# Optimization experiments

Hardware: AMD Instinct MI355X
Metric: run time of the kernel (lower is better)

Reference implementation:

```python
import jax, jax.numpy as jnp
import numpy as np

L, B, S, E, H, V = 4, 2, 1024, 1024, 16, 32000
HD = E // H          # head_size = 64
FF = 6 * E           # FeedForward expansion = 6
EPS = 1e-5


def setup_inputs() -> dict:
    key = jax.random.key(0)
    ks = jax.random.split(key, 12)
    std = jnp.float32(0.02)

    def nrm(k, shape):
        return jax.random.normal(k, shape, jnp.float32) * std

    return {
        "x":   jax.random.randint(ks[0], (B, S), 0, V),
        "emb": nrm(ks[1], (V, E)),            # token embedding table
        "pos": nrm(ks[2], (S, E)),            # position embedding table (context = S)
        "Wq":  nrm(ks[3], (L, H, E, HD)),     # per-layer, per-head q Linear (no bias)
        "Wk":  nrm(ks[4], (L, H, E, HD)),
        "Wv":  nrm(ks[5], (L, H, E, HD)),
        "Wo":  nrm(ks[6], (L, E, E)),         # MHA output projection
        "g1":  jnp.ones((L, E), jnp.float32), "b1": jnp.zeros((L, E), jnp.float32),
        "g2":  jnp.ones((L, E), jnp.float32), "b2": jnp.zeros((L, E), jnp.float32),
        "W1":  nrm(ks[7], (L, E, FF)),        # FFN up
        "W2":  nrm(ks[8], (L, FF, E)),        # FFN down
        "gf":  jnp.ones((E,), jnp.float32), "bf": jnp.zeros((E,), jnp.float32),
        "Wf":  nrm(ks[9], (E, V)),            # final LM head (no bias)
    }


def _ln(x, g, b):
    mu = jnp.mean(x, -1, keepdims=True)
    var = jnp.mean((x - mu) ** 2, -1, keepdims=True)
    return (x - mu) * jax.lax.rsqrt(var + EPS) * g + b


def _gpt(x, emb, pos, Wq, Wk, Wv, Wo, g1, b1, g2, b2, W1, W2, gf, bf, Wf):
    Bsz, Sl = x.shape
    h = emb[x] + pos[:Sl]                         # [B,S,E]
    mask = jnp.tril(jnp.ones((Sl, Sl), bool))     # causal 'trill' buffer

    def block(h, p):
        wq, wk, wv, wo, ga, ba, gb, bb, w1, w2 = p
        z = _ln(h, ga, ba)
        q = jnp.einsum('bse,hed->bhsd', z, wq)
        k = jnp.einsum('bse,hed->bhsd', z, wk)
        v = jnp.einsum('bse,hed->bhsd', z, wv)
        att = jnp.einsum('bhsd,bhtd->bhst', q, k) * (HD ** -0.5)
        att = jnp.where(mask, att, -jnp.inf)
        att = jax.nn.softmax(att, axis=-1)
        o = jnp.einsum('bhst,bhtd->bhsd', att, v)
        o = o.transpose(0, 2, 1, 3).reshape(h.shape[0], h.shape[1], E)  # concat heads
        h = h + o @ wo                                                   # residual 1
        z = _ln(h, gb, bb)
        h = h + jax.nn.gelu(z @ w1, approximate=False) @ w2              # residual 2
        return h, None

    h, _ = jax.lax.scan(block, h, (Wq, Wk, Wv, Wo, g1, b1, g2, b2, W1, W2))
    return _ln(h, gf, bf) @ Wf                    # logits [B,S,V]


def reference(x, emb, pos, Wq, Wk, Wv, Wo, g1, b1, g2, b2, W1, W2, gf, bf, Wf):
    return _gpt(x, emb, pos, Wq, Wk, Wv, Wo, g1, b1, g2, b2, W1, W2, gf, bf, Wf)
```

## Files before the change

kernel.cpp:

```cpp
#include <hip/hip_runtime.h>
#include <hip/hip_bf16.h>
#include <math.h>


typedef unsigned short ushort_t;
typedef unsigned short us8 __attribute__((ext_vector_type(8)));
typedef unsigned short us4 __attribute__((ext_vector_type(4)));
typedef __bf16 bf16x8 __attribute__((ext_vector_type(8)));
typedef float f32x4 __attribute__((ext_vector_type(4)));

#define LN_EPS 1e-5f

__device__ inline ushort_t f2bf(float f) {
    union { float f; unsigned u; } v; v.f = f;
    unsigned r = v.u + 0x7FFFu + ((v.u >> 16) & 1u);
    return (ushort_t)(r >> 16);
}

__device__ inline ushort_t bf16u(float f) {
    __hip_bfloat16 h = __float2bfloat16(f);
    return *(ushort_t*)&h;
}

#define GLD_LDS16(gp, lp)                                                  \
    __builtin_amdgcn_global_load_lds(                                      \
        (const __attribute__((address_space(1))) unsigned int*)(gp),       \
        (__attribute__((address_space(3))) unsigned int*)(lp), 16, 0, 0)

enum { EPI_F32 = 0, EPI_BF16 = 1, EPI_ADDF32 = 2, EPI_GELU = 3, EPI_TBF16 = 4,
       EPI_ATOM = 5, EPI_QKV = 6 };

template<int EPI>
__global__ __launch_bounds__(512)
void gemm8ph(const ushort_t* __restrict__ A, const ushort_t* __restrict__ B,
             void* __restrict__ Cv, int mt, int K, int lda, int ldb, int ldc)
{
    extern __shared__ ushort_t smem[];

    const int nwg  = gridDim.x;
    const int orig = blockIdx.x;
    int wgid = orig;
    if (nwg >= 8) {
        const int q = nwg >> 3, r = nwg & 7;
        const int xcd = orig & 7, i = orig >> 3;
        wgid = (xcd < r ? xcd * (q + 1) : r * (q + 1) + (xcd - r) * q) + i;
    }
    const int m0 = (wgid % mt) * 256;
    const int n0 = (wgid / mt) * 256;

    const int tid  = threadIdx.x;
    const int lane = tid & 63;
    const int wid  = tid >> 6;
    const int wm   = wid >> 2, wn = wid & 3;
    const int cg   = lane >> 4, cl = lane & 15;

    const int nt = K >> 6;
    const int ni = nt >> 1;

    auto stageA = [&](int t, int h) {
        ushort_t* dst = smem + (t & 1) * 32768 + h * 8192;
        const int k0 = t * 64;
        #pragma unroll
        for (int q = 0; q < 2; ++q) {
            const int slot = q * 512 + tid;
            const int r = slot >> 3, pc = slot & 7;
            const int col = (pc ^ (r & 7)) * 8;
            GLD_LDS16(&A[(long)(m0 + h * 128 + r) * lda + k0 + col], dst + slot * 8);
        }
    };
    auto stageB = [&](int t, int h) {
        ushort_t* dst = smem + (t & 1) * 32768 + 16384 + h * 8192;
        const int k0 = t * 64;
        #pragma unroll
        for (int q = 0; q < 2; ++q) {
            const int slot = q * 512 + tid;
            const int r = slot >> 3, pc = slot & 7;
            const int col = (pc ^ (r & 7)) * 8;
            GLD_LDS16(&B[(long)(n0 + h * 128 + r) * ldb + k0 + col], dst + slot * 8);
        }
    };

    stageA(0, 0); stageA(0, 1);
    stageB(0, 0); stageB(0, 1);
    stageB(1, 0); stageB(1, 1);
    asm volatile("s_waitcnt vmcnt(4)" ::: "memory");
    __builtin_amdgcn_s_barrier();

    f32x4 acc[8][4] = {};
    bf16x8 breg[4][2];

    for (int i = 0; i < ni; ++i) {
        const int te = 2 * i, to = te + 1;
        const bool nl = (i + 1 < ni);

        #pragma unroll
        for (int p = 0; p < 8; ++p) {
            const int t = (p < 4) ? te : to;
            const int q = p & 3;
            const ushort_t* Ar = smem + (t & 1) * 32768;
            const ushort_t* Br = Ar + 16384;

            if (q == 0) {
                #pragma unroll
                for (int nf = 0; nf < 4; ++nf) {
                    const int rb = wn * 64 + nf * 16 + cl;
                    #pragma unroll
                    for (int kk = 0; kk < 2; ++kk)
                        breg[nf][kk] = __builtin_bit_cast(bf16x8, *(const us8*)&Br[
                            rb * 64 + (((kk * 4 + cg) ^ (rb & 7)) * 8)]);
                }
            }
            bf16x8 af[2][2];
            #pragma unroll
            for (int mi = 0; mi < 2; ++mi) {
                const int ra = wm * 128 + q * 32 + mi * 16 + cl;
                #pragma unroll
                for (int kk = 0; kk < 2; ++kk)
                    af[mi][kk] = __builtin_bit_cast(bf16x8, *(const us8*)&Ar[
                        ra * 64 + (((kk * 4 + cg) ^ (ra & 7)) * 8)]);
            }

            if (p == 0)      { stageA(to, 0); }
            else if (p == 1) { stageA(to, 1); if (nl) stageB(te + 2, 0); }
            else if (p == 2) { if (nl) stageB(te + 2, 1); }
            else if (p == 4) { if (nl) stageA(te + 2, 0); }
            else if (p == 5) { if (nl) stageA(te + 2, 1); }
            else if (p == 6) { if (nl) stageB(to + 2, 0); }
            else if (p == 7) { if (nl) stageB(to + 2, 1); }

            __builtin_amdgcn_s_barrier();
            asm volatile("s_waitcnt lgkmcnt(0)" ::: "memory");
            __builtin_amdgcn_s_setprio(1);
            #pragma unroll
            for (int mi = 0; mi < 2; ++mi)
                #pragma unroll
                for (int nf = 0; nf < 4; ++nf)
                    #pragma unroll
                    for (int kk = 0; kk < 2; ++kk)
                        acc[q * 2 + mi][nf] = __builtin_amdgcn_mfma_f32_16x16x32_bf16(
                            af[mi][kk], breg[nf][kk], acc[q * 2 + mi][nf], 0, 0, 0);
            __builtin_amdgcn_s_setprio(0);

            if (p == 3) {
                if (nl) asm volatile("s_waitcnt vmcnt(4)" ::: "memory");
                else    asm volatile("s_waitcnt vmcnt(0)" ::: "memory");
            } else if (p == 7 && nl) {
                asm volatile("s_waitcnt vmcnt(4)" ::: "memory");
            }
            __builtin_amdgcn_s_barrier();
        }
    }

    if (EPI == EPI_F32) {
        float* lds_f = (float*)smem;
        #pragma unroll
        for (int c = 0; c < 2; ++c) {
            #pragma unroll
            for (int mf4 = 0; mf4 < 4; ++mf4) {
                #pragma unroll
                for (int nf = 0; nf < 4; ++nf) {
                    const int scol = (wn * 64 + nf * 16 + cl) ^ (cg << 4);
                    #pragma unroll
                    for (int r = 0; r < 4; ++r) {
                        const int lrow = wm * 64 + mf4 * 16 + cg * 4 + r;
                        lds_f[lrow * 256 + scol] = acc[c * 4 + mf4][nf][r];
                    }
                }
            }
            __builtin_amdgcn_s_barrier();
            #pragma unroll
            for (int rr = 0; rr < 16; ++rr) {
                const int lrow = wid * 16 + rr;
                const int rowg = m0 + (lrow >> 6) * 128 + c * 64 + (lrow & 63);
                const int lcol = (lane * 4) ^ ((((lrow >> 2) & 3)) << 4);
                const f32x4 v  = *(const f32x4*)&lds_f[lrow * 256 + lane * 4];
                *(f32x4*)&((float*)Cv)[(long)rowg * ldc + n0 + lcol] = v;
            }
            if (c == 0) __builtin_amdgcn_s_barrier();
        }
        return;
    }

    const int rb = m0 + wm * 128 + cg * 4;
    const int cb = n0 + wn * 64 + cl;

    #pragma unroll
    for (int mf = 0; mf < 8; ++mf) {
        #pragma unroll
        for (int nf = 0; nf < 4; ++nf) {
            const int colg = cb + nf * 16;
            #pragma unroll
            for (int r = 0; r < 4; ++r) {
                const int  rowg = rb + mf * 16 + r;
                const long off  = (long)rowg * ldc + colg;
                const float val = acc[mf][nf][r];
                if (EPI == EPI_GELU) {
                    float g = 0.5f * val * (1.0f + erff(val * 0.70710678118654752f));
                    ((ushort_t*)Cv)[off] = f2bf(g);
                } else {
                    ((ushort_t*)Cv)[off] = f2bf(val);
                }
            }
        }
    }
}

template<int EPI>
__global__ __launch_bounds__(512)
void gemm8p(const ushort_t* __restrict__ A, const ushort_t* __restrict__ B,
            void* __restrict__ Cv, int mt, int K, int lda, int ldb, int ldc,
            long bsA, long bsB, long bsC)
{
    extern __shared__ ushort_t smem[];

    const int nwg  = gridDim.x;
    const int orig = blockIdx.x;
    int wgid = orig;
    if (nwg >= 8) {
        const int q = nwg >> 3, r = nwg & 7;
        const int xcd = orig & 7, i = orig >> 3;
        wgid = (xcd < r ? xcd * (q + 1) : r * (q + 1) + (xcd - r) * q) + i;
    }
    const int m0 = (wgid % mt) * 128;
    const int n0 = (wgid / mt) * 256;

    A += (long)blockIdx.z * bsA;
    B += (long)blockIdx.z * bsB;

    const int tid  = threadIdx.x;
    const int lane = tid & 63;
    const int wid  = tid >> 6;
    const int wm   = wid >> 2, wn = wid & 3;
    const int cg   = lane >> 4, cl = lane & 15;
    const int lr   = lane >> 3;
    const int lcc  = (lane & 7) * 8;

    const int nt = K >> 6;

    auto stage = [&](int kt, int buf, int part) {
        ushort_t* base = smem + buf * 24576;
        const int k0 = kt * 64;
        if (part < 2) {
            const int rbase = part * 64 + wid * 8;
            const int row   = rbase + lr;
            const int col   = lcc ^ ((row & 7) << 3);
            GLD_LDS16(&A[(long)(m0 + row) * lda + k0 + col], base + rbase * 64);
        } else {
            const int rbase = (part - 2) * 64 + wid * 8;
            const int row   = rbase + lr;
            const int col   = lcc ^ ((row & 7) << 3);
            GLD_LDS16(&B[(long)(n0 + row) * ldb + k0 + col],
                      base + 8192 + rbase * 64);
        }
    };

    #pragma unroll
    for (int p = 0; p < 6; ++p) stage(0, 0, p);
    #pragma unroll
    for (int p = 0; p < 6; ++p) stage(1, 1, p);
    asm volatile("s_waitcnt vmcnt(6)" ::: "memory");
    __builtin_amdgcn_s_barrier();

    f32x4 acc[4][4] = {};

    for (int t = 0; t < nt; ++t) {
        const ushort_t* Aq = smem + (t % 3) * 24576;
        const ushort_t* Bq = Aq + 8192;
        const int sbuf = (t + 2) % 3;
        const bool do_stage = (t + 2 < nt);

        bf16x8 breg[4][2];
        #pragma unroll
        for (int p = 0; p < 4; ++p) {
            const int rowA = wm * 64 + p * 16 + cl;
            bf16x8 aA[2];
            #pragma unroll
            for (int kk = 0; kk < 2; ++kk)
                aA[kk] = __builtin_bit_cast(bf16x8, *(const us8*)&Aq[
                    rowA * 64 + ((kk * 32 + cg * 8) ^ ((rowA & 7) << 3))]);
            if (p == 0) {
                #pragma unroll
                for (int nj = 0; nj < 4; ++nj) {
                    const int rowB = wn * 64 + nj * 16 + cl;
                    #pragma unroll
                    for (int kk = 0; kk < 2; ++kk)
                        breg[nj][kk] = __builtin_bit_cast(bf16x8, *(const us8*)&Bq[
                            rowB * 64 + ((kk * 32 + cg * 8) ^ ((rowB & 7) << 3))]);
                }
            }
            if (do_stage) {
                if (p == 0)      { stage(t + 2, sbuf, 0); stage(t + 2, sbuf, 1); }
                else if (p == 1) { stage(t + 2, sbuf, 2); stage(t + 2, sbuf, 3); }
                else if (p == 2) { stage(t + 2, sbuf, 4); }
                else             { stage(t + 2, sbuf, 5); }
            }
            __builtin_amdgcn_s_setprio(1);
            #pragma unroll
            for (int nj = 0; nj < 4; ++nj)
                #pragma unroll
                for (int kk = 0; kk < 2; ++kk)
                    acc[p][nj] = __builtin_amdgcn_mfma_f32_16x16x32_bf16(
                        aA[kk], breg[nj][kk], acc[p][nj], 0, 0, 0);
            __builtin_amdgcn_s_setprio(0);
            __builtin_amdgcn_s_barrier();
        }
        if (do_stage) asm volatile("s_waitcnt vmcnt(6)" ::: "memory");
        else          asm volatile("s_waitcnt vmcnt(0)" ::: "memory");
        __builtin_amdgcn_s_barrier();
    }

    const int rb = m0 + wm * 64 + cg * 4;
    const int cb = n0 + wn * 64 + cl;

    #pragma unroll
    for (int mi = 0; mi < 4; ++mi) {
        #pragma unroll
        for (int nj = 0; nj < 4; ++nj) {
            const int colg = cb + nj * 16;
            if (EPI == EPI_QKV) {
                ushort_t* Q = (ushort_t*)Cv;
                if (n0 < 1024) {
                    #pragma unroll
                    for (int r = 0; r < 4; ++r)
                        Q[(long)(rb + mi * 16 + r) * 1024 + colg] = f2bf(acc[mi][nj][r]);
                } else if (n0 < 2048) {
                    #pragma unroll
                    for (int r = 0; r < 4; ++r)
                        Q[2097152 + (long)(rb + mi * 16 + r) * 1024 + (colg - 1024)] =
                            f2bf(acc[mi][nj][r]);
                } else {
                    ushort_t* Vt = Q + 4194304;
                    const int rowg = rb + mi * 16;
                    const long boff = (long)(rowg >> 10) * 1048576;
                    us4 o4;
                    #pragma unroll
                    for (int r = 0; r < 4; ++r) o4[r] = f2bf(acc[mi][nj][r]);
                    *(us4*)&Vt[boff + (long)(colg - 2048) * 1024 + (rowg & 1023)] = o4;
                }
            } else {
                #pragma unroll
                for (int r = 0; r < 4; ++r) {
                    const int  rowg = rb + mi * 16 + r;
                    const long off  = (long)rowg * ldc + colg;
                    const float val = acc[mi][nj][r];
                    if (EPI == EPI_F32) {
                        ((float*)Cv)[off] = val;
                    } else if (EPI == EPI_GELU) {
                        float g = 0.5f * val * (1.0f + erff(val * 0.70710678118654752f));
                        ((ushort_t*)Cv)[off] = f2bf(g);
                    } else if (EPI == EPI_ATOM) {
                        atomicAdd(&((float*)Cv)[off], val);
                    } else {
                        ((ushort_t*)Cv)[off] = f2bf(val);
                    }
                }
            }
        }
    }
}

template<int EPI, int MT>
__global__ __launch_bounds__(256)
void gemm128(const ushort_t* __restrict__ A, const ushort_t* __restrict__ B,
             void* __restrict__ Cv, int K, int lda, int ldb, int ldc)
{
    const int m0 = blockIdx.x * (MT * 32);
    const int n0 = blockIdx.y * 128;

    __shared__ __align__(16) ushort_t As[MT * 32][64];
    __shared__ __align__(16) ushort_t Bs[128][64];

    const int tid  = threadIdx.x;
    const int lane = tid & 63;
    const int wid  = tid >> 6;
    const int wr   = wid >> 1, wc = wid & 1;
    const int lr   = lane >> 3;
    const int lc   = (lane & 7) * 8;
    const int cg   = lane >> 4;
    const int cl   = lane & 15;

    f32x4 acc[MT][4] = {};

    for (int k0 = 0; k0 < K; k0 += 64) {
        #pragma unroll
        for (int j = 0; j < MT; ++j) {
            const int r = wid * (8 * MT) + j * 8;
            GLD_LDS16(&A[(long)(m0 + r + lr) * lda + k0 + lc], &As[r][0]);
        }
        #pragma unroll
        for (int j = 0; j < 4; ++j) {
            const int r = wid * 32 + j * 8;
            GLD_LDS16(&B[(long)(n0 + r + lr) * ldb + k0 + lc], &Bs[r][0]);
        }
        __syncthreads();
        #pragma unroll
        for (int kk = 0; kk < 2; ++kk) {
            const int krd = kk * 32 + cg * 8;
            bf16x8 af[MT], bfr[4];
            #pragma unroll
            for (int mi = 0; mi < MT; ++mi)
                af[mi] = __builtin_bit_cast(bf16x8,
                    *(const us8*)&As[wr * (MT * 16) + mi * 16 + cl][krd]);
            #pragma unroll
            for (int nj = 0; nj < 4; ++nj)
                bfr[nj] = __builtin_bit_cast(bf16x8,
                    *(const us8*)&Bs[wc * 64 + nj * 16 + cl][krd]);
            #pragma unroll
            for (int mi = 0; mi < MT; ++mi)
                #pragma unroll
                for (int nj = 0; nj < 4; ++nj)
                    acc[mi][nj] = __builtin_amdgcn_mfma_f32_16x16x32_bf16(
                        af[mi], bfr[nj], acc[mi][nj], 0, 0, 0);
        }
        __syncthreads();
    }

    const int rb = m0 + wr * (MT * 16) + cg * 4;
    const int cb = n0 + wc * 64 + cl;

    #pragma unroll
    for (int mi = 0; mi < MT; ++mi)
        #pragma unroll
        for (int nj = 0; nj < 4; ++nj)
            #pragma unroll
            for (int r = 0; r < 4; ++r) {
                const long off = (long)(rb + mi * 16 + r) * ldc + cb + nj * 16;
                const float val = acc[mi][nj][r];
                if (EPI == EPI_ADDF32)      ((float*)Cv)[off] += val;
                else if (EPI == EPI_F32)    ((float*)Cv)[off] = val;
                else                        ((ushort_t*)Cv)[off] = f2bf(val);
            }
}

#define ATT_SCL 0.1803368805f
#define ATT_THR 12.0f

__global__ __launch_bounds__(256)
void flash_attn(const ushort_t* __restrict__ qb, const ushort_t* __restrict__ kb,
                const ushort_t* __restrict__ vT, ushort_t* __restrict__ ob)
{
    const int qt = gridDim.x - 1 - blockIdx.x;
    const int hh = blockIdx.y;
    const int bb = blockIdx.z;
    const int lane = threadIdx.x & 63;
    const int w    = threadIdx.x >> 6;
    const int cg   = lane >> 4;
    const int cl   = lane & 15;

    __shared__ __align__(16) ushort_t P_lds[4][16][72];

    const int q0 = qt * 64;
    const long tokQ = (long)bb * 1024 + q0 + w * 16 + cl;

    bf16x8 qf[2];
    #pragma unroll
    for (int kk = 0; kk < 2; ++kk)
        qf[kk] = __builtin_bit_cast(bf16x8,
            *(const us8*)&qb[tokQ * 1024 + hh * 64 + kk * 32 + cg * 8]);

    const ushort_t* kbase = kb + (long)bb * 1048576 + hh * 64;
    const ushort_t* vbase = vT + (long)bb * 1048576 + (long)hh * 65536;

    f32x4 o[4] = {};
    float m4[4], l4[4];
    #pragma unroll
    for (int r = 0; r < 4; ++r) { m4[r] = -1e30f; l4[r] = 0.0f; }

    for (int tt = 0; tt <= qt; ++tt) {
        const int t0 = tt * 64;
        f32x4 s[4] = {};
        __builtin_amdgcn_s_setprio(1);
        #pragma unroll
        for (int nj = 0; nj < 4; ++nj) {
            const ushort_t* kp = kbase + (long)(t0 + nj * 16 + cl) * 1024 + cg * 8;
            bf16x8 kf0 = __builtin_bit_cast(bf16x8, *(const us8*)kp);
            bf16x8 kf1 = __builtin_bit_cast(bf16x8, *(const us8*)(kp + 32));
            s[nj] = __builtin_amdgcn_mfma_f32_16x16x32_bf16(qf[0], kf0, s[nj], 0, 0, 0);
            s[nj] = __builtin_amdgcn_mfma_f32_16x16x32_bf16(qf[1], kf1, s[nj], 0, 0, 0);
        }
        __builtin_amdgcn_s_setprio(0);

        bf16x8 vreg[4][2];
        #pragma unroll
        for (int nj = 0; nj < 4; ++nj) {
            const ushort_t* vp = vbase + (long)(nj * 16 + cl) * 1024 + t0 + cg * 8;
            vreg[nj][0] = __builtin_bit_cast(bf16x8, *(const us8*)vp);
            vreg[nj][1] = __builtin_bit_cast(bf16x8, *(const us8*)(vp + 32));
        }

        const bool diag = (tt == qt);
        float pm[4] = {-3e30f, -3e30f, -3e30f, -3e30f};
        #pragma unroll
        for (int nj = 0; nj < 4; ++nj)
            #pragma unroll
            for (int r = 0; r < 4; ++r) {
                float v = s[nj][r] * ATT_SCL;
                if (diag && (t0 + nj * 16 + cl) > (q0 + w * 16 + cg * 4 + r))
                    v = -3e30f;
                s[nj][r] = v;
                pm[r] = fmaxf(pm[r], v);
            }
        #pragma unroll
        for (int r = 0; r < 4; ++r)
            #pragma unroll
            for (int msk = 1; msk < 16; msk <<= 1)
                pm[r] = fmaxf(pm[r], __shfl_xor(pm[r], msk));

        const bool grow = (pm[0] > m4[0] + ATT_THR) || (pm[1] > m4[1] + ATT_THR)
                       || (pm[2] > m4[2] + ATT_THR) || (pm[3] > m4[3] + ATT_THR);
        if (__any(grow)) {
            #pragma unroll
            for (int r = 0; r < 4; ++r) {
                const float mn = fmaxf(m4[r], pm[r]);
                const float al = __builtin_amdgcn_exp2f(m4[r] - mn);
                m4[r] = mn;
                l4[r] *= al;
                #pragma unroll
                for (int nj = 0; nj < 4; ++nj) o[nj][r] *= al;
            }
        }
        float ps[4] = {0.0f, 0.0f, 0.0f, 0.0f};
        #pragma unroll
        for (int nj = 0; nj < 4; ++nj)
            #pragma unroll
            for (int r = 0; r < 4; ++r) {
                const float p = __builtin_amdgcn_exp2f(s[nj][r] - m4[r]);
                s[nj][r] = p;
                ps[r] += p;
            }
        #pragma unroll
        for (int r = 0; r < 4; ++r) {
            #pragma unroll
            for (int msk = 1; msk < 16; msk <<= 1)
                ps[r] += __shfl_xor(ps[r], msk);
            l4[r] += ps[r];
        }
        #pragma unroll
        for (int nj = 0; nj < 4; ++nj)
            #pragma unroll
            for (int r = 0; r < 4; ++r)
                P_lds[w][cg * 4 + r][nj * 16 + cl] = bf16u(s[nj][r]);
        asm volatile("s_waitcnt lgkmcnt(0)" ::: "memory");
        __builtin_amdgcn_sched_barrier(0);
        bf16x8 pa[2];
        #pragma unroll
        for (int kk = 0; kk < 2; ++kk)
            pa[kk] = __builtin_bit_cast(bf16x8,
                *(const us8*)&P_lds[w][cl][kk * 32 + cg * 8]);
        __builtin_amdgcn_s_setprio(1);
        #pragma unroll
        for (int nj = 0; nj < 4; ++nj) {
            o[nj] = __builtin_amdgcn_mfma_f32_16x16x32_bf16(pa[0], vreg[nj][0], o[nj], 0, 0, 0);
            o[nj] = __builtin_amdgcn_mfma_f32_16x16x32_bf16(pa[1], vreg[nj][1], o[nj], 0, 0, 0);
        }
        __builtin_amdgcn_s_setprio(0);
    }

    #pragma unroll
    for (int r = 0; r < 4; ++r) {
        const float inv = 1.0f / l4[r];
        const long tok = (long)bb * 1024 + q0 + w * 16 + cg * 4 + r;
        #pragma unroll
        for (int nj = 0; nj < 4; ++nj)
            ob[tok * 1024 + hh * 64 + nj * 16 + cl] = bf16u(o[nj][r] * inv);
    }
}

__global__ __launch_bounds__(256)
void transpose_conv(const float* __restrict__ in, ushort_t* __restrict__ out,
                    long ldin, long ldout, long bsin, long bsout,
                    long bsout_hi, int zmod)
{
    __shared__ float tile[32][132];
    const int tx = threadIdx.x, ty = threadIdx.y;
    const long bin  = (long)blockIdx.z * bsin;
    const long bout = (long)(blockIdx.z % zmod) * bsout
                    + (long)(blockIdx.z / zmod) * bsout_hi;
    const int n0 = blockIdx.x * 32, k0 = blockIdx.y * 128;
    #pragma unroll
    for (int i = 0; i < 16; ++i)
        tile[tx][ty + i * 8] = in[bin + (long)(k0 + ty + i * 8) * ldin + n0 + tx];
    __syncthreads();
    #pragma unroll
    for (int i = 0; i < 4; ++i) {
        const int n = ty + i * 8;
        const f32x4 v = *(const f32x4*)&tile[n][tx * 4];
        us4 o4;
        o4[0] = bf16u(v[0]); o4[1] = bf16u(v[1]);
        o4[2] = bf16u(v[2]); o4[3] = bf16u(v[3]);
        *(us4*)&out[bout + (long)(n0 + n) * ldout + k0 + tx * 4] = o4;
    }
}

__global__ __launch_bounds__(256)
void embed_kernel(const int* __restrict__ x, const float* __restrict__ emb,
                  const float* __restrict__ pos, float* __restrict__ h)
{
    const int row = blockIdx.x, tid = threadIdx.x;
    const int s = row & 1023;
    const int idx = x[row];
    const float4 e = ((const float4*)(emb + (long)idx * 1024))[tid];
    const float4 p = ((const float4*)(pos + (long)s * 1024))[tid];
    float4 o; o.x = e.x + p.x; o.y = e.y + p.y; o.z = e.z + p.z; o.w = e.w + p.w;
    ((float4*)(h + (long)row * 1024))[tid] = o;
}

__global__ __launch_bounds__(256)
void ln_kernel(const float* __restrict__ x, const float* __restrict__ g,
               const float* __restrict__ b, ushort_t* __restrict__ z)
{
    const int row = blockIdx.x, tid = threadIdx.x;
    const float4 v = ((const float4*)(x + (long)row * 1024))[tid];
    float s  = v.x + v.y + v.z + v.w;
    float sq = v.x * v.x + v.y * v.y + v.z * v.z + v.w * v.w;
    #pragma unroll
    for (int o = 32; o > 0; o >>= 1) { s += __shfl_down(s, o); sq += __shfl_down(sq, o); }
    __shared__ float ls[4], lq[4];
    if ((tid & 63) == 0) { ls[tid >> 6] = s; lq[tid >> 6] = sq; }
    __syncthreads();
    s  = ls[0] + ls[1] + ls[2] + ls[3];
    sq = lq[0] + lq[1] + lq[2] + lq[3];
    const float mu   = s * (1.0f / 1024.0f);
    const float var  = sq * (1.0f / 1024.0f) - mu * mu;
    const float rstd = rsqrtf(var + LN_EPS);
    const float4 gg = ((const float4*)g)[tid];
    const float4 bb = ((const float4*)b)[tid];
    us4 o4;
    o4[0] = f2bf((v.x - mu) * rstd * gg.x + bb.x);
    o4[1] = f2bf((v.y - mu) * rstd * gg.y + bb.y);
    o4[2] = f2bf((v.z - mu) * rstd * gg.z + bb.z);
    o4[3] = f2bf((v.w - mu) * rstd * gg.w + bb.w);
    *(us4*)(z + (long)row * 1024 + tid * 4) = o4;
}

extern "C" void kernel_launch(void* const* d_in, const int* in_sizes, int n_in,
                              void* d_out, int out_size, void* d_ws, size_t ws_size,
                              hipStream_t stream)
{
    const int*   x   = (const int*)  d_in[0];
    const float* emb = (const float*)d_in[1];
    const float* pos = (const float*)d_in[2];
    const float* Wq  = (const float*)d_in[3];
    const float* Wk  = (const float*)d_in[4];
    const float* Wv  = (const float*)d_in[5];
    const float* Wo  = (const float*)d_in[6];
    const float* g1  = (const float*)d_in[7];
    const float* b1  = (const float*)d_in[8];
    const float* g2  = (const float*)d_in[9];
    const float* b2  = (const float*)d_in[10];
    const float* W1  = (const float*)d_in[11];
    const float* W2  = (const float*)d_in[12];
    const float* gf  = (const float*)d_in[13];
    const float* bfp = (const float*)d_in[14];
    const float* Wf  = (const float*)d_in[15];
    float* out = (float*)d_out;

    char* ws = (char*)d_ws;
    size_t off = 0;
    auto alloc = [&](size_t bytes) {
        char* p = ws + off;
        off = (off + bytes + 255) & ~(size_t)255;
        return p;
    };
    ushort_t* WqkvT = (ushort_t*)alloc(4UL * 3145728 * 2);
    ushort_t* WoT   = (ushort_t*)alloc(4UL * 1048576 * 2);
    ushort_t* W1T   = (ushort_t*)alloc(4UL * 6291456 * 2);
    ushort_t* W2T   = (ushort_t*)alloc(4UL * 6291456 * 2);
    ushort_t* WfT   = (ushort_t*)alloc(32768000UL * 2);
    float*    h     = (float*)   alloc(2048UL * 1024 * 4);
    ushort_t* z     = (ushort_t*)alloc(2048UL * 1024 * 2);
    ushort_t* qb    = (ushort_t*)alloc(3UL * 2048 * 1024 * 2);
    ushort_t* kb    = qb + 2097152;
    ushort_t* vT    = qb + 4194304;
    ushort_t* ob    = (ushort_t*)alloc(2048UL * 1024 * 2);
    ushort_t* ub    = (ushort_t*)alloc(2048UL * 6144 * 2);
    (void)ws_size; (void)in_sizes; (void)n_in; (void)out_size;

    const int LDS8P = 2 * 32768 * 2;
    const int LDS3B = 3 * 49152;
    hipFuncSetAttribute((const void*)&gemm8ph<EPI_F32>,
                        hipFuncAttributeMaxDynamicSharedMemorySize, LDS8P);
    hipFuncSetAttribute((const void*)&gemm8ph<EPI_GELU>,
                        hipFuncAttributeMaxDynamicSharedMemorySize, LDS8P);
    hipFuncSetAttribute((const void*)&gemm8p<EPI_QKV>,
                        hipFuncAttributeMaxDynamicSharedMemorySize, LDS3B);
    hipFuncSetAttribute((const void*)&gemm8p<EPI_ATOM>,
                        hipFuncAttributeMaxDynamicSharedMemorySize, LDS3B);

    const dim3 tb(32, 8);
    transpose_conv<<<dim3(2,   8, 64), tb, 0, stream>>>(Wq, WqkvT,           64, 1024, 65536, 65536, 3145728, 16);
    transpose_conv<<<dim3(2,   8, 64), tb, 0, stream>>>(Wk, WqkvT + 1048576, 64, 1024, 65536, 65536, 3145728, 16);
    transpose_conv<<<dim3(2,   8, 64), tb, 0, stream>>>(Wv, WqkvT + 2097152, 64, 1024, 65536, 65536, 3145728, 16);
    transpose_conv<<<dim3(32,  8,  4), tb, 0, stream>>>(Wo, WoT, 1024,  1024, 1048576, 1048576, 0, 4);
    transpose_conv<<<dim3(192, 8,  4), tb, 0, stream>>>(W1, W1T, 6144,  1024, 6291456, 6291456, 0, 4);
    transpose_conv<<<dim3(32, 48,  4), tb, 0, stream>>>(W2, W2T, 1024,  6144, 6291456, 6291456, 0, 4);
    transpose_conv<<<dim3(1000,8,  1), tb, 0, stream>>>(Wf, WfT, 32000, 1024, 0,       0,       0, 1);

    embed_kernel<<<2048, 256, 0, stream>>>(x, emb, pos, h);

    for (int l = 0; l < 4; ++l) {
        const size_t wff = (size_t)l * 6291456;

        ln_kernel<<<2048, 256, 0, stream>>>(h, g1 + l * 1024, b1 + l * 1024, z);

        gemm8p<EPI_QKV><<<dim3(16 * 12), 512, LDS3B, stream>>>(
            z, WqkvT + (size_t)l * 3145728, qb, 16, 1024, 1024, 1024, 1024, 0, 0, 0);

        flash_attn<<<dim3(16, 16, 2), 256, 0, stream>>>(qb, kb, vT, ob);

        gemm128<EPI_ADDF32, 2><<<dim3(32, 8), 256, 0, stream>>>(
            ob, WoT + (size_t)l * 1048576, h, 1024, 1024, 1024, 1024);

        ln_kernel<<<2048, 256, 0, stream>>>(h, g2 + l * 1024, b2 + l * 1024, z);

        gemm8ph<EPI_GELU><<<dim3(8 * 24), 512, LDS8P, stream>>>(
            z, W1T + wff, ub, 8, 1024, 1024, 1024, 6144);
        gemm8p<EPI_ATOM><<<dim3(16 * 4, 1, 4), 512, LDS3B, stream>>>(
            ub, W2T + wff, h, 16, 1536, 6144, 6144, 1024, 1536, 1536, 0);
    }

    ln_kernel<<<2048, 256, 0, stream>>>(h, gf, bfp, z);
    gemm8ph<EPI_F32><<<dim3(8 * 125), 512, LDS8P, stream>>>(
        z, WfT, out, 8, 1024, 1024, 1024, 32000);
}
```

Baseline: 1.168 ms.

## Replace split-K atomics and residual adds with partial buffers reduced in LayerNorm

The W2 split-K GEMM now writes four fp32 partial results to separate buffers instead of atomically adding into the residual stream. The Wo projection writes to its own buffer instead of adding into h. The following LayerNorm kernel sums the partials into h and then normalizes, which removes atomic contention and folds the residual adds into an existing pass. In exchange it costs extra workspace and extra partial-buffer traffic in the LN kernel.

```diff
diff --git a/kernel.cpp b/kernel.cpp
--- a/kernel.cpp
+++ b/kernel.cpp
@@ -344,12 +344,10 @@
                     const long off  = (long)rowg * ldc + colg;
                     const float val = acc[mi][nj][r];
                     if (EPI == EPI_F32) {
-                        ((float*)Cv)[off] = val;
+                        ((float*)Cv)[(long)blockIdx.z * bsC + off] = val;
                     } else if (EPI == EPI_GELU) {
                         float g = 0.5f * val * (1.0f + erff(val * 0.70710678118654752f));
                         ((ushort_t*)Cv)[off] = f2bf(g);
-                    } else if (EPI == EPI_ATOM) {
-                        atomicAdd(&((float*)Cv)[off], val);
                     } else {
                         ((ushort_t*)Cv)[off] = f2bf(val);
                     }
@@ -605,12 +603,22 @@
     ((float4*)(h + (long)row * 1024))[tid] = o;
 }
 
+template<int NP>
 __global__ __launch_bounds__(256)
-void ln_kernel(const float* __restrict__ x, const float* __restrict__ g,
-               const float* __restrict__ b, ushort_t* __restrict__ z)
+void ln_red_kernel(float* __restrict__ h, const float* __restrict__ part,
+                   long pstride, const float* __restrict__ g,
+                   const float* __restrict__ b, ushort_t* __restrict__ z)
 {
     const int row = blockIdx.x, tid = threadIdx.x;
-    const float4 v = ((const float4*)(x + (long)row * 1024))[tid];
+    const long roff = (long)row * 1024 + tid * 4;
+    float4 v = *(const float4*)&h[roff];
+    #pragma unroll
+    for (int p = 0; p < NP; ++p) {
+        const float4 a = *(const float4*)&part[p * pstride + roff];
+        v.x += a.x; v.y += a.y; v.z += a.z; v.w += a.w;
+    }
+    if (NP > 0) *(float4*)&h[roff] = v;
+
     float s  = v.x + v.y + v.z + v.w;
     float sq = v.x * v.x + v.y * v.y + v.z * v.z + v.w * v.w;
     #pragma unroll
@@ -630,7 +638,7 @@
     o4[1] = f2bf((v.y - mu) * rstd * gg.y + bb.y);
     o4[2] = f2bf((v.z - mu) * rstd * gg.z + bb.z);
     o4[3] = f2bf((v.w - mu) * rstd * gg.w + bb.w);
-    *(us4*)(z + (long)row * 1024 + tid * 4) = o4;
+    *(us4*)&z[roff] = o4;
 }
 
 extern "C" void kernel_launch(void* const* d_in, const int* in_sizes, int n_in,
@@ -674,6 +682,8 @@
     ushort_t* vT    = qb + 4194304;
     ushort_t* ob    = (ushort_t*)alloc(2048UL * 1024 * 2);
     ushort_t* ub    = (ushort_t*)alloc(2048UL * 6144 * 2);
+    float*    wob   = (float*)   alloc(2048UL * 1024 * 4);
+    float*    fp    = (float*)   alloc(4UL * 2048 * 1024 * 4);
     (void)ws_size; (void)in_sizes; (void)n_in; (void)out_size;
 
     const int LDS8P = 2 * 32768 * 2;
@@ -684,7 +694,7 @@
                         hipFuncAttributeMaxDynamicSharedMemorySize, LDS8P);
     hipFuncSetAttribute((const void*)&gemm8p<EPI_QKV>,
                         hipFuncAttributeMaxDynamicSharedMemorySize, LDS3B);
-    hipFuncSetAttribute((const void*)&gemm8p<EPI_ATOM>,
+    hipFuncSetAttribute((const void*)&gemm8p<EPI_F32>,
                         hipFuncAttributeMaxDynamicSharedMemorySize, LDS3B);
 
     const dim3 tb(32, 8);
@@ -701,25 +711,31 @@
     for (int l = 0; l < 4; ++l) {
         const size_t wff = (size_t)l * 6291456;
 
-        ln_kernel<<<2048, 256, 0, stream>>>(h, g1 + l * 1024, b1 + l * 1024, z);
+        if (l == 0)
+            ln_red_kernel<0><<<2048, 256, 0, stream>>>(
+                h, fp, 2097152, g1, b1, z);
+        else
+            ln_red_kernel<4><<<2048, 256, 0, stream>>>(
+                h, fp, 2097152, g1 + l * 1024, b1 + l * 1024, z);
 
         gemm8p<EPI_QKV><<<dim3(16 * 12), 512, LDS3B, stream>>>(
             z, WqkvT + (size_t)l * 3145728, qb, 16, 1024, 1024, 1024, 1024, 0, 0, 0);
 
         flash_attn<<<dim3(16, 16, 2), 256, 0, stream>>>(qb, kb, vT, ob);
 
-        gemm128<EPI_ADDF32, 2><<<dim3(32, 8), 256, 0, stream>>>(
-            ob, WoT + (size_t)l * 1048576, h, 1024, 1024, 1024, 1024);
-
-        ln_kernel<<<2048, 256, 0, stream>>>(h, g2 + l * 1024, b2 + l * 1024, z);
+        gemm128<EPI_F32, 2><<<dim3(32, 8), 256, 0, stream>>>(
+            ob, WoT + (size_t)l * 1048576, wob, 1024, 1024, 1024, 1024);
+
+        ln_red_kernel<1><<<2048, 256, 0, stream>>>(
+            h, wob, 0, g2 + l * 1024, b2 + l * 1024, z);
 
         gemm8ph<EPI_GELU><<<dim3(8 * 24), 512, LDS8P, stream>>>(
             z, W1T + wff, ub, 8, 1024, 1024, 1024, 6144);
-        gemm8p<EPI_ATOM><<<dim3(16 * 4, 1, 4), 512, LDS3B, stream>>>(
-            ub, W2T + wff, h, 16, 1536, 6144, 6144, 1024, 1536, 1536, 0);
-    }
-
-    ln_kernel<<<2048, 256, 0, stream>>>(h, gf, bfp, z);
+        gemm8p<EPI_F32><<<dim3(16 * 4, 1, 4), 512, LDS3B, stream>>>(
+            ub, W2T + wff, fp, 16, 1536, 6144, 6144, 1024, 1536, 1536, 2097152);
+    }
+
+    ln_red_kernel<4><<<2048, 256, 0, stream>>>(h, fp, 2097152, gf, bfp, z);
     gemm8ph<EPI_F32><<<dim3(8 * 125), 512, LDS8P, stream>>>(
         z, WfT, out, 8, 1024, 1024, 1024, 32000);
 }
```

Result: faster. 1.110 ms (-5.0%).
